# Performance work log

Measured on AMD Instinct MI355X. Metric: run time of the kernel, lower is better.

## Reference

```python
import jax, jax.numpy as jnp
import numpy as np

IN_FEATURES = 3
NUM_FREQUENCIES = 10  # in_features == 3 branch of PosEncoding
OUT_DIM = IN_FEATURES + 2 * IN_FEATURES * NUM_FREQUENCIES  # 63


def setup_inputs() -> dict:
    key = jax.random.key(0)
    coords = jax.random.uniform(key, (1, 2097152, IN_FEATURES), dtype=jnp.float32)
    return {"coords": coords}


def reference(coords) -> jnp.ndarray:
    # coords: [B, N, D] with D = IN_FEATURES
    B = coords.shape[0]
    c = coords.reshape(B, -1, IN_FEATURES)
    # freqs[i] = 2^i * pi, i = 0..NUM_FREQUENCIES-1
    freqs = (2.0 ** jnp.arange(NUM_FREQUENCIES, dtype=coords.dtype)) * jnp.pi
    # angles: [B, N, F, D]  (freq axis before feature axis to match the
    # original loop order: for i in freqs: for j in features: sin, cos)
    ang = c[:, :, None, :] * freqs[None, None, :, None]
    # [B, N, F, D, 2] -> flatten to [B, N, 2*F*D] in (i, j, sin/cos) order
    sc = jnp.stack([jnp.sin(ang), jnp.cos(ang)], axis=-1)
    sc = sc.reshape(B, c.shape[1], 2 * NUM_FREQUENCIES * IN_FEATURES)
    return jnp.concatenate([c, sc], axis=-1)  # [B, N, OUT_DIM]
```

## Files before the change

kernel.cpp:

```cpp
#include <hip/hip_runtime.h>


#define NPTS_PER_BLOCK 256
#define OUT_PER_POINT  63
#define TILE_FLOATS    (NPTS_PER_BLOCK * OUT_PER_POINT)
#define TILE_V4        (TILE_FLOATS / 4)

__global__ __launch_bounds__(256) void posenc_kernel(
    const float* __restrict__ coords,
    float4* __restrict__ out4,
    int n_points)
{
    __shared__ float4 lds4[TILE_V4];
    float* lds = (float*)lds4;

    const int t = (int)threadIdx.x;
    const int p = (int)blockIdx.x * NPTS_PER_BLOCK + t;

    if (p < n_points) {
        const float c0 = coords[p * 3 + 0];
        const float c1 = coords[p * 3 + 1];
        const float c2 = coords[p * 3 + 2];

        float* o = &lds[t * OUT_PER_POINT];
        o[0] = c0; o[1] = c1; o[2] = c2;

        float r0 = c0 * 0.5f, r1 = c1 * 0.5f, r2 = c2 * 0.5f;

        int k = 3;
        #pragma unroll
        for (int i = 0; i < 10; ++i) {
            const float f0 = r0 - floorf(r0);
            const float f1 = r1 - floorf(r1);
            const float f2 = r2 - floorf(r2);
            o[k + 0] = __builtin_amdgcn_sinf(f0);
            o[k + 1] = __builtin_amdgcn_cosf(f0);
            o[k + 2] = __builtin_amdgcn_sinf(f1);
            o[k + 3] = __builtin_amdgcn_cosf(f1);
            o[k + 4] = __builtin_amdgcn_sinf(f2);
            o[k + 5] = __builtin_amdgcn_cosf(f2);
            k += 6;
            r0 *= 2.0f; r1 *= 2.0f; r2 *= 2.0f;
        }
    }
    __syncthreads();

    const int gbase = (int)blockIdx.x * TILE_V4;
    for (int v = t; v < TILE_V4; v += NPTS_PER_BLOCK) {
        out4[gbase + v] = lds4[v];
    }
}

extern "C" void kernel_launch(void* const* d_in, const int* in_sizes, int n_in,
                              void* d_out, int out_size, void* d_ws, size_t ws_size,
                              hipStream_t stream) {
    const float* coords = (const float*)d_in[0];
    float4* out4 = (float4*)d_out;

    const int n_points = in_sizes[0] / 3;
    const int grid = (n_points + NPTS_PER_BLOCK - 1) / NPTS_PER_BLOCK;

    posenc_kernel<<<grid, NPTS_PER_BLOCK, 0, stream>>>(coords, out4, n_points);
}
```

Measured before the change: 106.4 us.

## Stage output per wave to drop block barrier and use nontemporal stores

Each wave now owns its own 64-point slice of the LDS tile and copies it out to global memory itself, so the block-wide __syncthreads is removed. Global writes switch to nontemporal stores, which bypass cache retention for the streaming output, and a bounds check against the total output size is added. The change relies on LDS visibility within a wave without an explicit wave barrier. That is usually safe on AMD hardware but depends on compiler ordering.

```diff
diff --git a/kernel.cpp b/kernel.cpp
--- a/kernel.cpp
+++ b/kernel.cpp
@@ -1,28 +1,34 @@
 #include <hip/hip_runtime.h>
 
 
-#define NPTS_PER_BLOCK 256
+typedef float f32x4 __attribute__((ext_vector_type(4)));
+
+#define BLOCK_THREADS  256
+#define WAVE_PTS       64
 #define OUT_PER_POINT  63
-#define TILE_FLOATS    (NPTS_PER_BLOCK * OUT_PER_POINT)
-#define TILE_V4        (TILE_FLOATS / 4)
+#define WAVE_FLOATS    (WAVE_PTS * OUT_PER_POINT)
+#define WAVE_V4        (WAVE_FLOATS / 4)
+#define BLOCK_V4       (WAVE_V4 * (BLOCK_THREADS / 64))
 
-__global__ __launch_bounds__(256) void posenc_kernel(
+__global__ __launch_bounds__(BLOCK_THREADS) void posenc_kernel(
     const float* __restrict__ coords,
-    float4* __restrict__ out4,
+    f32x4* __restrict__ out4,
     int n_points)
 {
-    __shared__ float4 lds4[TILE_V4];
+    __shared__ f32x4 lds4[BLOCK_V4];
     float* lds = (float*)lds4;
 
-    const int t = (int)threadIdx.x;
-    const int p = (int)blockIdx.x * NPTS_PER_BLOCK + t;
+    const int t    = (int)threadIdx.x;
+    const int wave = t >> 6;
+    const int lane = t & 63;
+    const int p    = (int)blockIdx.x * BLOCK_THREADS + t;
 
     if (p < n_points) {
         const float c0 = coords[p * 3 + 0];
         const float c1 = coords[p * 3 + 1];
         const float c2 = coords[p * 3 + 2];
 
-        float* o = &lds[t * OUT_PER_POINT];
+        float* o = &lds[(wave * WAVE_PTS + lane) * OUT_PER_POINT];
         o[0] = c0; o[1] = c1; o[2] = c2;
 
         float r0 = c0 * 0.5f, r1 = c1 * 0.5f, r2 = c2 * 0.5f;
@@ -43,11 +49,17 @@
             r0 *= 2.0f; r1 *= 2.0f; r2 *= 2.0f;
         }
     }
-    __syncthreads();
 
-    const int gbase = (int)blockIdx.x * TILE_V4;
-    for (int v = t; v < TILE_V4; v += NPTS_PER_BLOCK) {
-        out4[gbase + v] = lds4[v];
+    const long long gbase = (long long)blockIdx.x * BLOCK_V4 + wave * WAVE_V4;
+    const long long gmax  = (long long)n_points * OUT_PER_POINT / 4;
+    const int lbase = wave * WAVE_V4;
+
+    #pragma unroll
+    for (int it = 0; it < (WAVE_V4 + 63) / 64; ++it) {
+        const int v = it * 64 + lane;
+        if (v < WAVE_V4 && gbase + v < gmax) {
+            __builtin_nontemporal_store(lds4[lbase + v], &out4[gbase + v]);
+        }
     }
 }
 
@@ -55,10 +67,10 @@
                               void* d_out, int out_size, void* d_ws, size_t ws_size,
                               hipStream_t stream) {
     const float* coords = (const float*)d_in[0];
-    float4* out4 = (float4*)d_out;
+    f32x4* out4 = (f32x4*)d_out;
 
     const int n_points = in_sizes[0] / 3;
-    const int grid = (n_points + NPTS_PER_BLOCK - 1) / NPTS_PER_BLOCK;
+    const int grid = (n_points + BLOCK_THREADS - 1) / BLOCK_THREADS;
 
-    posenc_kernel<<<grid, NPTS_PER_BLOCK, 0, stream>>>(coords, out4, n_points);
+    posenc_kernel<<<grid, BLOCK_THREADS, 0, stream>>>(coords, out4, n_points);
 }
```

Result: faster. 101.6 us (-4.5%).
